# Kernel tuning notes

Measured on AMD Instinct MI355X. Metric: run time of the kernel, lower is better.

The kernel has to match this reference:

```python
import jax, jax.numpy as jnp
import numpy as np

B, C, N, H = 16, 512, 4096, 512  # batch, visual_channels, visual_flat, hidden_size


def setup_inputs() -> dict:
    key = jax.random.key(0)
    kx, k1, k2, k3, k4 = jax.random.split(key, 5)
    stdv = 1.0 / np.sqrt(H)  # reset_parameters: uniform(-1/sqrt(size(0)), ...), size(0)=H for all weights
    u = lambda k, shape: jax.random.uniform(k, shape, jnp.float32, -stdv, stdv)
    return {
        "visual_inputs": jax.random.normal(kx, (B, C, N), jnp.float32),
        "w_cf": u(k1, (H, N)),  # channel_f: Linear(visual_flat -> hidden)
        "w_cg": u(k2, (H, N)),  # channel_g
        "w_sf": u(k3, (H, C)),  # spatial_f: Conv1d(C -> H, k=1), squeezed
        "w_sg": u(k4, (H, C)),  # spatial_g
    }


def reference(visual_inputs, w_cf, w_cg, w_sf, w_sg):
    x = visual_inputs  # [B, C, N]
    # ---- channel branch: sim[b,c,c'] = <cf[b,c,:], cg[b,c',:]>; summed over dim c then softmax over c'
    cf = jnp.einsum('bcn,hn->bch', x, w_cf)          # [B, C, H]
    cg = jnp.einsum('bcn,hn->bch', x, w_cg)          # [B, C, H]
    # sum_c sim[b,c,c'] = (sum_c cf[b,c,:]) . cg[b,c',:]  -- avoids [B,C,C]
    ch_comp = jnp.einsum('bh,bch->bc', cf.sum(axis=1), cg)        # [B, C]
    channel_mask = jax.nn.softmax(ch_comp, axis=1)[:, :, None]     # [B, C, 1]
    # ---- spatial branch: sim[b,i,j] = <sf[b,:,i], sg[b,:,j]>; summed over dim i then softmax over j
    sf = jnp.einsum('bcn,hc->bhn', x, w_sf)          # [B, H, N]
    sg = jnp.einsum('bcn,hc->bhn', x, w_sg)          # [B, H, N]
    sp_comp = jnp.einsum('bh,bhn->bn', sf.sum(axis=2), sg)         # [B, N]
    spatial_mask = jax.nn.softmax(sp_comp, axis=1)[:, None, :]     # [B, 1, N]
    outputs = x * channel_mask * spatial_mask        # [B, C, N]
    return outputs, channel_mask, spatial_mask
```

## Files before the change

kernel.cpp:

```cpp
#include <hip/hip_runtime.h>

#define Bq 16
#define Cq 512
#define Nq 4096
#define Hq 512

__global__ __launch_bounds__(256) void k1_stats(const float* __restrict__ x,
                                                float* __restrict__ xs_n,
                                                float* __restrict__ xs_c){
  __shared__ float red[4][256];
  int blk = blockIdx.x;
  if (blk < 256){
    int b    = blk >> 4;
    int nc   = blk & 15;
    int wave = threadIdx.x >> 6;
    int lane = threadIdx.x & 63;
    const float* p = x + (size_t)b*Cq*Nq + (nc << 8) + (lane << 2);
    float4 acc = {0.f,0.f,0.f,0.f};
    #pragma unroll 8
    for (int c = wave; c < Cq; c += 4){
      float4 v = *(const float4*)(p + (size_t)c*Nq);
      acc.x += v.x; acc.y += v.y; acc.z += v.z; acc.w += v.w;
    }
    *(float4*)&red[wave][lane << 2] = acc;
    __syncthreads();
    int t = threadIdx.x;
    float s = (red[0][t] + red[1][t]) + (red[2][t] + red[3][t]);
    xs_n[(size_t)b*Nq + (nc << 8) + t] = s;
  } else {
    int blk2 = blk - 256;
    int b = blk2 >> 9;
    int c = blk2 & 511;
    const float4* row = (const float4*)(x + ((size_t)b*Cq + c)*Nq);
    float acc = 0.f;
    #pragma unroll
    for (int s = 0; s < 4; ++s){
      float4 v = row[s*256 + threadIdx.x];
      acc += (v.x + v.y) + (v.z + v.w);
    }
    #pragma unroll
    for (int off=32; off; off>>=1) acc += __shfl_down(acc, off, 64);
    if ((threadIdx.x & 63) == 0) red[threadIdx.x >> 6][0] = acc;
    __syncthreads();
    if (threadIdx.x == 0)
      xs_c[(size_t)b*Cq + c] = (red[0][0]+red[1][0])+(red[2][0]+red[3][0]);
  }
}

__global__ __launch_bounds__(256) void k2_s(const float* __restrict__ w_cf,
                                            const float* __restrict__ w_sf,
                                            const float* __restrict__ xs_n,
                                            const float* __restrict__ xs_c,
                                            float* __restrict__ s_cf,
                                            float* __restrict__ s_sf){
  __shared__ float red[4][Bq];
  int blk = blockIdx.x;
  const float* w; const float* src; float* dst; int L;
  if (blk < Hq) { w = w_cf + (size_t)blk*Nq; src = xs_n; dst = s_cf; L = Nq; }
  else          { w = w_sf + (size_t)(blk-Hq)*Cq; src = xs_c; dst = s_sf; L = Cq; }
  int h = blk & (Hq-1);
  int t = threadIdx.x;
  int wave = t >> 6, lane = t & 63;
  float acc[Bq];
  #pragma unroll
  for (int b=0;b<Bq;b++) acc[b]=0.f;
  for (int i0 = t*4; i0 < L; i0 += 1024){
    float4 wv = *(const float4*)(w + i0);
    #pragma unroll
    for (int b=0;b<Bq;b++){
      float4 sv = *(const float4*)(src + (size_t)b*L + i0);
      acc[b] += wv.x*sv.x + wv.y*sv.y + wv.z*sv.z + wv.w*sv.w;
    }
  }
  #pragma unroll
  for (int b=0;b<Bq;b++){
    float v = acc[b];
    #pragma unroll
    for (int off=32; off; off>>=1) v += __shfl_down(v, off, 64);
    if (lane == 0) red[wave][b] = v;
  }
  __syncthreads();
  if (t < Bq)
    dst[(size_t)t*Hq + h] = (red[0][t]+red[1][t])+(red[2][t]+red[3][t]);
}

__global__ __launch_bounds__(256) void k3_v(const float* __restrict__ w_cg,
                                            const float* __restrict__ w_sg,
                                            const float* __restrict__ s_cf,
                                            const float* __restrict__ s_sf,
                                            float* __restrict__ part_cg,
                                            float* __restrict__ part_sg){
  __shared__ float sl[Bq*64];
  int blk = blockIdx.x;
  const float* w; const float* s; float* dst; int L, jc, hc;
  if (blk < 128){ w=w_cg; s=s_cf; dst=part_cg; L=Nq; jc=blk>>3; hc=blk&7; }
  else { int k=blk-128; w=w_sg; s=s_sf; dst=part_sg; L=Cq; jc=k>>3; hc=k&7; }
  int h0 = hc*64;
  for (int i = threadIdx.x; i < Bq*64; i += 256){
    int b = i >> 6, hh = i & 63;
    sl[i] = s[b*Hq + h0 + hh];
  }
  __syncthreads();
  int j = (jc<<8) + (int)threadIdx.x;
  float acc[Bq];
  #pragma unroll
  for (int b=0;b<Bq;b++) acc[b]=0.f;
  for (int hh=0; hh<64; ++hh){
    float wv = w[(size_t)(h0+hh)*L + j];
    #pragma unroll
    for (int b=0;b<Bq;b++) acc[b] += sl[b*64+hh]*wv;
  }
  #pragma unroll
  for (int b=0;b<Bq;b++) dst[((size_t)hc*Bq + b)*L + j] = acc[b];
}

__global__ __launch_bounds__(256) void k3b_red(const float* __restrict__ part_cg,
                                               const float* __restrict__ part_sg,
                                               float* __restrict__ v_cg,
                                               float* __restrict__ v_sg){
  int blk = blockIdx.x;
  if (blk < 256){
    int i = (blk << 8) + (int)threadIdx.x;
    float acc = 0.f;
    #pragma unroll
    for (int hc=0; hc<8; ++hc) acc += part_cg[(size_t)hc*(Bq*Nq) + i];
    v_cg[i] = acc;
  } else {
    int i = ((blk-256) << 8) + (int)threadIdx.x;
    float acc = 0.f;
    #pragma unroll
    for (int hc=0; hc<8; ++hc) acc += part_sg[(size_t)hc*(Bq*Cq) + i];
    v_sg[i] = acc;
  }
}

__global__ __launch_bounds__(256) void k4_comp(const float* __restrict__ x,
                                               const float* __restrict__ v_cg,
                                               const float* __restrict__ v_sg,
                                               float* __restrict__ sp,
                                               float* __restrict__ ch){
  __shared__ float red[4][256];
  int blk = blockIdx.x;
  if (blk < 256){
    int b    = blk >> 4;
    int nc   = blk & 15;
    int wave = threadIdx.x >> 6;
    int lane = threadIdx.x & 63;
    const float* p  = x + (size_t)b*Cq*Nq + (nc << 8) + (lane << 2);
    const float* vs = v_sg + (size_t)b*Cq;
    float4 acc = {0.f,0.f,0.f,0.f};
    #pragma unroll 8
    for (int c = wave; c < Cq; c += 4){
      float4 v = *(const float4*)(p + (size_t)c*Nq);
      float s = vs[c];
      acc.x += v.x*s; acc.y += v.y*s; acc.z += v.z*s; acc.w += v.w*s;
    }
    *(float4*)&red[wave][lane << 2] = acc;
    __syncthreads();
    int t = threadIdx.x;
    float s = (red[0][t] + red[1][t]) + (red[2][t] + red[3][t]);
    sp[(size_t)b*Nq + (nc << 8) + t] = s;
  } else {
    int blk2 = blk - 256;
    int b = blk2 >> 9;
    int c = blk2 & 511;
    const float4* row = (const float4*)(x + ((size_t)b*Cq + c)*Nq);
    const float4* vg  = (const float4*)(v_cg + (size_t)b*Nq);
    float acc = 0.f;
    #pragma unroll
    for (int s = 0; s < 4; ++s){
      float4 xv = row[s*256 + threadIdx.x];
      float4 vv = vg [s*256 + threadIdx.x];
      acc += xv.x*vv.x + xv.y*vv.y + xv.z*vv.z + xv.w*vv.w;
    }
    #pragma unroll
    for (int off=32; off; off>>=1) acc += __shfl_down(acc, off, 64);
    if ((threadIdx.x & 63) == 0) red[threadIdx.x >> 6][0] = acc;
    __syncthreads();
    if (threadIdx.x == 0)
      ch[(size_t)b*Cq + c] = (red[0][0]+red[1][0])+(red[2][0]+red[3][0]);
  }
}

__global__ __launch_bounds__(256) void k5_softmax(const float* __restrict__ ch,
                                                  const float* __restrict__ sp,
                                                  float* __restrict__ out){
  __shared__ float lds[4];
  __shared__ float bcast;
  int blk = blockIdx.x;
  const float* src; float* dst; int L;
  const size_t OUT0 = (size_t)Bq*Cq*Nq;
  if (blk < Bq){ int b=blk;    src=ch+(size_t)b*Cq; dst=out+OUT0+(size_t)b*Cq; L=Cq; }
  else         { int b=blk-Bq; src=sp+(size_t)b*Nq; dst=out+OUT0+(size_t)Bq*Cq+(size_t)b*Nq; L=Nq; }
  float m = -3.4e38f;
  for (int i=threadIdx.x;i<L;i+=256) m = fmaxf(m, src[i]);
  #pragma unroll
  for (int off=32; off; off>>=1) m = fmaxf(m, __shfl_down(m, off, 64));
  if ((threadIdx.x&63)==0) lds[threadIdx.x>>6]=m;
  __syncthreads();
  if (threadIdx.x==0) bcast = fmaxf(fmaxf(lds[0],lds[1]),fmaxf(lds[2],lds[3]));
  __syncthreads();
  m = bcast;
  float ssum=0.f;
  for (int i=threadIdx.x;i<L;i+=256) ssum += __expf(src[i]-m);
  #pragma unroll
  for (int off=32; off; off>>=1) ssum += __shfl_down(ssum, off, 64);
  __syncthreads();
  if ((threadIdx.x&63)==0) lds[threadIdx.x>>6]=ssum;
  __syncthreads();
  if (threadIdx.x==0) bcast = 1.f/((lds[0]+lds[1])+(lds[2]+lds[3]));
  __syncthreads();
  float inv = bcast;
  for (int i=threadIdx.x;i<L;i+=256) dst[i] = __expf(src[i]-m)*inv;
}

__global__ __launch_bounds__(256) void k6_out(const float* __restrict__ x,
                                              float* __restrict__ out){
  const size_t OUT0 = (size_t)Bq*Cq*Nq;
  const float* cm = out + OUT0;
  const float* sm = out + OUT0 + (size_t)Bq*Cq;
  int blk = blockIdx.x;
  int b = blk >> 11;
  int r = blk & 2047;
  int c = r >> 2;
  int q = r & 3;
  size_t rowoff = ((size_t)b*Cq + c)*Nq;
  int n0 = q*1024 + (int)threadIdx.x*4;
  float4 xv = *(const float4*)(x + rowoff + n0);
  float4 sv = *(const float4*)(sm + (size_t)b*Nq + n0);
  float cmv = cm[b*Cq + c];
  float4 o;
  o.x = xv.x*cmv*sv.x; o.y = xv.y*cmv*sv.y;
  o.z = xv.z*cmv*sv.z; o.w = xv.w*cmv*sv.w;
  *(float4*)(out + rowoff + n0) = o;
}

extern "C" void kernel_launch(void* const* d_in, const int* in_sizes, int n_in,
                              void* d_out, int out_size, void* d_ws, size_t ws_size,
                              hipStream_t stream){
  const float* x    = (const float*)d_in[0];
  const float* w_cf = (const float*)d_in[1];
  const float* w_cg = (const float*)d_in[2];
  const float* w_sf = (const float*)d_in[3];
  const float* w_sg = (const float*)d_in[4];
  float* out = (float*)d_out;

  float* ws      = (float*)d_ws;
  float* xs_n    = ws;
  float* xs_c    = xs_n    + Bq*Nq;
  float* s_cf    = xs_c    + Bq*Cq;
  float* s_sf    = s_cf    + Bq*Hq;
  float* part_cg = s_sf    + Bq*Hq;
  float* part_sg = part_cg + 8*Bq*Nq;
  float* v_cg    = part_sg + 8*Bq*Cq;
  float* v_sg    = v_cg    + Bq*Nq;
  float* chc     = v_sg    + Bq*Cq;
  float* spc     = chc     + Bq*Cq;

  k1_stats  <<<256 + Bq*Cq, 256, 0, stream>>>(x, xs_n, xs_c);
  k2_s      <<<2*Hq,        256, 0, stream>>>(w_cf, w_sf, xs_n, xs_c, s_cf, s_sf);
  k3_v      <<<144,         256, 0, stream>>>(w_cg, w_sg, s_cf, s_sf, part_cg, part_sg);
  k3b_red   <<<288,         256, 0, stream>>>(part_cg, part_sg, v_cg, v_sg);
  k4_comp   <<<256 + Bq*Cq, 256, 0, stream>>>(x, v_cg, v_sg, spc, chc);
  k5_softmax<<<2*Bq,        256, 0, stream>>>(chc, spc, out);
  k6_out    <<<Bq*Cq*4,     256, 0, stream>>>(x, out);
}
```

Measured before the change: 356.7 us.

## Fuse row and column reductions of x into single-pass tiled kernels with partial sums

The stats kernel and the comp kernel each previously read x twice, once for column sums over channels and once for row sums over positions. Each now reads x once per tile and produces both the row and column reductions, writing partials that a new reduce kernel (k1b_red) or the softmax kernel combine. The softmax kernel now sums the partials into shared memory before normalising. The cost is an extra launch, per-iteration wave shuffles, and partial buffers that reuse one workspace arena.

```diff
diff --git a/kernel.cpp b/kernel.cpp
--- a/kernel.cpp
+++ b/kernel.cpp
@@ -6,44 +6,53 @@
 #define Hq 512
 
 __global__ __launch_bounds__(256) void k1_stats(const float* __restrict__ x,
-                                                float* __restrict__ xs_n,
-                                                float* __restrict__ xs_c){
+                                                float* __restrict__ part_xs_n,
+                                                float* __restrict__ part_xs_c){
   __shared__ float red[4][256];
+  int blk  = blockIdx.x;
+  int b    = blk >> 6;
+  int nc   = (blk >> 2) & 15;
+  int cq   = blk & 3;
+  int wave = threadIdx.x >> 6;
+  int lane = threadIdx.x & 63;
+  int c0   = cq*128 + wave;
+  const float* p = x + ((size_t)b*Cq + c0)*Nq + (nc << 8) + (lane << 2);
+  float* pc = part_xs_c + ((size_t)(b*16 + nc) << 9) + c0;
+  float4 acc = {0.f,0.f,0.f,0.f};
+  #pragma unroll 8
+  for (int k = 0; k < 32; ++k){
+    float4 v = *(const float4*)(p + (size_t)(k*4)*Nq);
+    acc.x += v.x; acc.y += v.y; acc.z += v.z; acc.w += v.w;
+    float r = (v.x + v.y) + (v.z + v.w);
+    #pragma unroll
+    for (int off=32; off; off>>=1) r += __shfl_down(r, off, 64);
+    if (lane == 0) pc[k*4] = r;
+  }
+  *(float4*)&red[wave][lane << 2] = acc;
+  __syncthreads();
+  int t = threadIdx.x;
+  part_xs_n[((size_t)(cq*Bq) + b)*Nq + (nc << 8) + t] =
+      (red[0][t] + red[1][t]) + (red[2][t] + red[3][t]);
+}
+
+__global__ __launch_bounds__(256) void k1b_red(const float* __restrict__ part_xs_n,
+                                               const float* __restrict__ part_xs_c,
+                                               float* __restrict__ xs_n,
+                                               float* __restrict__ xs_c){
   int blk = blockIdx.x;
   if (blk < 256){
-    int b    = blk >> 4;
-    int nc   = blk & 15;
-    int wave = threadIdx.x >> 6;
-    int lane = threadIdx.x & 63;
-    const float* p = x + (size_t)b*Cq*Nq + (nc << 8) + (lane << 2);
-    float4 acc = {0.f,0.f,0.f,0.f};
-    #pragma unroll 8
-    for (int c = wave; c < Cq; c += 4){
-      float4 v = *(const float4*)(p + (size_t)c*Nq);
-      acc.x += v.x; acc.y += v.y; acc.z += v.z; acc.w += v.w;
-    }
-    *(float4*)&red[wave][lane << 2] = acc;
-    __syncthreads();
-    int t = threadIdx.x;
-    float s = (red[0][t] + red[1][t]) + (red[2][t] + red[3][t]);
-    xs_n[(size_t)b*Nq + (nc << 8) + t] = s;
+    int i = (blk << 8) + (int)threadIdx.x;
+    float acc = 0.f;
+    #pragma unroll
+    for (int cq=0; cq<4; ++cq) acc += part_xs_n[(size_t)cq*(Bq*Nq) + i];
+    xs_n[i] = acc;
   } else {
-    int blk2 = blk - 256;
-    int b = blk2 >> 9;
-    int c = blk2 & 511;
-    const float4* row = (const float4*)(x + ((size_t)b*Cq + c)*Nq);
-    float acc = 0.f;
-    #pragma unroll
-    for (int s = 0; s < 4; ++s){
-      float4 v = row[s*256 + threadIdx.x];
-      acc += (v.x + v.y) + (v.z + v.w);
-    }
-    #pragma unroll
-    for (int off=32; off; off>>=1) acc += __shfl_down(acc, off, 64);
-    if ((threadIdx.x & 63) == 0) red[threadIdx.x >> 6][0] = acc;
-    __syncthreads();
-    if (threadIdx.x == 0)
-      xs_c[(size_t)b*Cq + c] = (red[0][0]+red[1][0])+(red[2][0]+red[3][0]);
+    int j = ((blk-256) << 8) + (int)threadIdx.x;
+    int b = j >> 9, c = j & 511;
+    float acc = 0.f;
+    #pragma unroll
+    for (int nc=0; nc<16; ++nc) acc += part_xs_c[((size_t)(b*16+nc) << 9) + c];
+    xs_c[j] = acc;
   }
 }
 
@@ -137,81 +146,88 @@
 __global__ __launch_bounds__(256) void k4_comp(const float* __restrict__ x,
                                                const float* __restrict__ v_cg,
                                                const float* __restrict__ v_sg,
-                                               float* __restrict__ sp,
-                                               float* __restrict__ ch){
+                                               float* __restrict__ part_sp,
+                                               float* __restrict__ part_ch){
   __shared__ float red[4][256];
-  int blk = blockIdx.x;
-  if (blk < 256){
-    int b    = blk >> 4;
-    int nc   = blk & 15;
-    int wave = threadIdx.x >> 6;
-    int lane = threadIdx.x & 63;
-    const float* p  = x + (size_t)b*Cq*Nq + (nc << 8) + (lane << 2);
-    const float* vs = v_sg + (size_t)b*Cq;
-    float4 acc = {0.f,0.f,0.f,0.f};
-    #pragma unroll 8
-    for (int c = wave; c < Cq; c += 4){
-      float4 v = *(const float4*)(p + (size_t)c*Nq);
-      float s = vs[c];
-      acc.x += v.x*s; acc.y += v.y*s; acc.z += v.z*s; acc.w += v.w*s;
-    }
-    *(float4*)&red[wave][lane << 2] = acc;
-    __syncthreads();
-    int t = threadIdx.x;
-    float s = (red[0][t] + red[1][t]) + (red[2][t] + red[3][t]);
-    sp[(size_t)b*Nq + (nc << 8) + t] = s;
-  } else {
-    int blk2 = blk - 256;
-    int b = blk2 >> 9;
-    int c = blk2 & 511;
-    const float4* row = (const float4*)(x + ((size_t)b*Cq + c)*Nq);
-    const float4* vg  = (const float4*)(v_cg + (size_t)b*Nq);
-    float acc = 0.f;
-    #pragma unroll
-    for (int s = 0; s < 4; ++s){
-      float4 xv = row[s*256 + threadIdx.x];
-      float4 vv = vg [s*256 + threadIdx.x];
-      acc += xv.x*vv.x + xv.y*vv.y + xv.z*vv.z + xv.w*vv.w;
-    }
-    #pragma unroll
-    for (int off=32; off; off>>=1) acc += __shfl_down(acc, off, 64);
-    if ((threadIdx.x & 63) == 0) red[threadIdx.x >> 6][0] = acc;
-    __syncthreads();
-    if (threadIdx.x == 0)
-      ch[(size_t)b*Cq + c] = (red[0][0]+red[1][0])+(red[2][0]+red[3][0]);
-  }
-}
-
-__global__ __launch_bounds__(256) void k5_softmax(const float* __restrict__ ch,
-                                                  const float* __restrict__ sp,
+  int blk  = blockIdx.x;
+  int b    = blk >> 6;
+  int nc   = (blk >> 2) & 15;
+  int cq   = blk & 3;
+  int wave = threadIdx.x >> 6;
+  int lane = threadIdx.x & 63;
+  int c0   = cq*128 + wave;
+  const float* p  = x + ((size_t)b*Cq + c0)*Nq + (nc << 8) + (lane << 2);
+  const float* vs = v_sg + (size_t)b*Cq + c0;
+  float4 g = *(const float4*)(v_cg + (size_t)b*Nq + (nc << 8) + (lane << 2));
+  float* pc = part_ch + ((size_t)(b*16 + nc) << 9) + c0;
+  float4 acc = {0.f,0.f,0.f,0.f};
+  #pragma unroll 8
+  for (int k = 0; k < 32; ++k){
+    float4 v = *(const float4*)(p + (size_t)(k*4)*Nq);
+    float s = vs[k*4];
+    acc.x += v.x*s; acc.y += v.y*s; acc.z += v.z*s; acc.w += v.w*s;
+    float r = v.x*g.x + v.y*g.y + v.z*g.z + v.w*g.w;
+    #pragma unroll
+    for (int off=32; off; off>>=1) r += __shfl_down(r, off, 64);
+    if (lane == 0) pc[k*4] = r;
+  }
+  *(float4*)&red[wave][lane << 2] = acc;
+  __syncthreads();
+  int t = threadIdx.x;
+  part_sp[((size_t)(cq*Bq) + b)*Nq + (nc << 8) + t] =
+      (red[0][t] + red[1][t]) + (red[2][t] + red[3][t]);
+}
+
+__global__ __launch_bounds__(256) void k5_softmax(const float* __restrict__ part_ch,
+                                                  const float* __restrict__ part_sp,
                                                   float* __restrict__ out){
+  __shared__ float buf[Nq];
   __shared__ float lds[4];
   __shared__ float bcast;
   int blk = blockIdx.x;
-  const float* src; float* dst; int L;
+  int t = threadIdx.x;
+  float* dst; int L;
   const size_t OUT0 = (size_t)Bq*Cq*Nq;
-  if (blk < Bq){ int b=blk;    src=ch+(size_t)b*Cq; dst=out+OUT0+(size_t)b*Cq; L=Cq; }
-  else         { int b=blk-Bq; src=sp+(size_t)b*Nq; dst=out+OUT0+(size_t)Bq*Cq+(size_t)b*Nq; L=Nq; }
+  if (blk < Bq){
+    int b = blk; L = Cq;
+    for (int c = t; c < Cq; c += 256){
+      float s = 0.f;
+      #pragma unroll
+      for (int nc=0; nc<16; ++nc) s += part_ch[((size_t)(b*16+nc) << 9) + c];
+      buf[c] = s;
+    }
+    dst = out + OUT0 + (size_t)b*Cq;
+  } else {
+    int b = blk - Bq; L = Nq;
+    for (int n = t; n < Nq; n += 256){
+      float s = 0.f;
+      #pragma unroll
+      for (int cq=0; cq<4; ++cq) s += part_sp[((size_t)(cq*Bq)+b)*Nq + n];
+      buf[n] = s;
+    }
+    dst = out + OUT0 + (size_t)Bq*Cq + (size_t)b*Nq;
+  }
+  __syncthreads();
   float m = -3.4e38f;
-  for (int i=threadIdx.x;i<L;i+=256) m = fmaxf(m, src[i]);
+  for (int i=t;i<L;i+=256) m = fmaxf(m, buf[i]);
   #pragma unroll
   for (int off=32; off; off>>=1) m = fmaxf(m, __shfl_down(m, off, 64));
-  if ((threadIdx.x&63)==0) lds[threadIdx.x>>6]=m;
-  __syncthreads();
-  if (threadIdx.x==0) bcast = fmaxf(fmaxf(lds[0],lds[1]),fmaxf(lds[2],lds[3]));
+  if ((t&63)==0) lds[t>>6]=m;
+  __syncthreads();
+  if (t==0) bcast = fmaxf(fmaxf(lds[0],lds[1]),fmaxf(lds[2],lds[3]));
   __syncthreads();
   m = bcast;
   float ssum=0.f;
-  for (int i=threadIdx.x;i<L;i+=256) ssum += __expf(src[i]-m);
+  for (int i=t;i<L;i+=256) ssum += __expf(buf[i]-m);
   #pragma unroll
   for (int off=32; off; off>>=1) ssum += __shfl_down(ssum, off, 64);
   __syncthreads();
-  if ((threadIdx.x&63)==0) lds[threadIdx.x>>6]=ssum;
-  __syncthreads();
-  if (threadIdx.x==0) bcast = 1.f/((lds[0]+lds[1])+(lds[2]+lds[3]));
+  if ((t&63)==0) lds[t>>6]=ssum;
+  __syncthreads();
+  if (t==0) bcast = 1.f/((lds[0]+lds[1])+(lds[2]+lds[3]));
   __syncthreads();
   float inv = bcast;
-  for (int i=threadIdx.x;i<L;i+=256) dst[i] = __expf(src[i]-m)*inv;
+  for (int i=t;i<L;i+=256) dst[i] = __expf(buf[i]-m)*inv;
 }
 
 __global__ __launch_bounds__(256) void k6_out(const float* __restrict__ x,
@@ -245,23 +261,27 @@
   const float* w_sg = (const float*)d_in[4];
   float* out = (float*)d_out;
 
-  float* ws      = (float*)d_ws;
-  float* xs_n    = ws;
-  float* xs_c    = xs_n    + Bq*Nq;
-  float* s_cf    = xs_c    + Bq*Cq;
-  float* s_sf    = s_cf    + Bq*Hq;
-  float* part_cg = s_sf    + Bq*Hq;
-  float* part_sg = part_cg + 8*Bq*Nq;
-  float* v_cg    = part_sg + 8*Bq*Cq;
-  float* v_sg    = v_cg    + Bq*Nq;
-  float* chc     = v_sg    + Bq*Cq;
-  float* spc     = chc     + Bq*Cq;
-
-  k1_stats  <<<256 + Bq*Cq, 256, 0, stream>>>(x, xs_n, xs_c);
-  k2_s      <<<2*Hq,        256, 0, stream>>>(w_cf, w_sf, xs_n, xs_c, s_cf, s_sf);
-  k3_v      <<<144,         256, 0, stream>>>(w_cg, w_sg, s_cf, s_sf, part_cg, part_sg);
-  k3b_red   <<<288,         256, 0, stream>>>(part_cg, part_sg, v_cg, v_sg);
-  k4_comp   <<<256 + Bq*Cq, 256, 0, stream>>>(x, v_cg, v_sg, spc, chc);
-  k5_softmax<<<2*Bq,        256, 0, stream>>>(chc, spc, out);
-  k6_out    <<<Bq*Cq*4,     256, 0, stream>>>(x, out);
-}
+  float* ws = (float*)d_ws;
+  float* xs_n = ws;
+  float* xs_c = xs_n + Bq*Nq;
+  float* s_cf = xs_c + Bq*Cq;
+  float* s_sf = s_cf + Bq*Hq;
+  float* v_cg = s_sf + Bq*Hq;
+  float* v_sg = v_cg + Bq*Nq;
+  float* arena = v_sg + Bq*Cq;
+  float* part_xs_n = arena;
+  float* part_xs_c = arena + 4*Bq*Nq;
+  float* part_cg   = arena;
+  float* part_sg   = arena + 8*Bq*Nq;
+  float* part_sp   = arena;
+  float* part_ch   = arena + 4*Bq*Nq;
+
+  k1_stats  <<<1024,    256, 0, stream>>>(x, part_xs_n, part_xs_c);
+  k1b_red   <<<288,     256, 0, stream>>>(part_xs_n, part_xs_c, xs_n, xs_c);
+  k2_s      <<<2*Hq,    256, 0, stream>>>(w_cf, w_sf, xs_n, xs_c, s_cf, s_sf);
+  k3_v      <<<144,     256, 0, stream>>>(w_cg, w_sg, s_cf, s_sf, part_cg, part_sg);
+  k3b_red   <<<288,     256, 0, stream>>>(part_cg, part_sg, v_cg, v_sg);
+  k4_comp   <<<1024,    256, 0, stream>>>(x, v_cg, v_sg, part_sp, part_ch);
+  k5_softmax<<<2*Bq,    256, 0, stream>>>(part_ch, part_sp, out);
+  k6_out    <<<Bq*Cq*4, 256, 0, stream>>>(x, out);
+}
```

After: 322.7 us. 1.11x faster.
